# Kernel tuning notes

Measured on AMD Instinct MI355X. Metric: run time of the kernel, lower is better.

## Reference

```python
import jax, jax.numpy as jnp
import numpy as np

N, D_IN, D_OUT, H, E = 8192, 1024, 1024, 1024, 8
EPS = 0.2
S_FACTOR = 5.0


def setup_inputs() -> dict:
    key = jax.random.key(0)
    k0, k1, k2, k3 = jax.random.split(key, 4)
    x = jax.random.normal(k0, (N, D_IN), jnp.float32)
    # selector Linear(nIn, E); weights scaled by sFactor as in SMoE.__init__
    Wsel = jax.random.normal(k1, (D_IN, E), jnp.float32) * (S_FACTOR / np.sqrt(D_IN))
    bsel = jnp.zeros((E,), jnp.float32)
    # stacked 2-layer MLP experts: Linear(D_IN,H) -> ReLU -> Linear(H,D_OUT)
    W1 = jax.random.normal(k2, (E, D_IN, H), jnp.float32) / np.sqrt(D_IN)
    b1 = jnp.zeros((E, H), jnp.float32)
    W2 = jax.random.normal(k3, (E, H, D_OUT), jnp.float32) / np.sqrt(H)
    b2 = jnp.zeros((E, D_OUT), jnp.float32)
    return {"x": x, "Wsel": Wsel, "bsel": bsel, "W1": W1, "b1": b1, "W2": W2, "b2": b2}


def _sparse_weights(weightMat):
    # sort experts per token, descending (torch.sort(..., 1, descending=True))
    order = jnp.argsort(-weightMat, axis=1)                # [N,E]
    topW = jnp.take_along_axis(weightMat, order, axis=1)
    cumW = jnp.cumsum(topW, axis=1)
    capped = jnp.minimum(cumW, 1.0 - EPS)
    sw_sorted = jax.nn.relu(capped - cumW + topW)          # sparse weights, sorted order
    # softCost (side-effect metric in the original; not returned by SMoE.forward)
    shifted = jnp.pad(sw_sorted[:, 1:], ((0, 0), (0, 1)))
    _soft_cost = jnp.sum(jnp.where(shifted > 0, 1.0, sw_sorted), axis=1)
    # faithful to torch.gather(sparse_weight, 1, index) in the source
    sw = jnp.take_along_axis(sw_sorted, order, axis=1)     # [N,E]
    return sw


def reference(x, Wsel, bsel, W1, b1, W2, b2):
    weightMat = jax.nn.softmax(x @ Wsel + bsel, axis=1)    # [N,E] selector
    sw = _sparse_weights(weightMat)                        # [N,E] sparse combine weights
    # dense (vectorized) expert dispatch: tokens with sw==0 contribute 0,
    # numerically identical to the gather/scatter_add loop in sparse_MoE
    h = jax.nn.relu(jnp.einsum('nd,edh->enh', x, W1) + b1[:, None, :])   # [E,N,H]
    y = jnp.einsum('enh,eho->eno', h, W2) + b2[:, None, :]               # [E,N,O]
    out = jnp.einsum('ne,eno->no', sw, y)                                # [N,O]
    return out
```

## Files before the change

kernel.cpp:

```cpp
#include <hip/hip_runtime.h>
#include <hip/hip_bf16.h>
#include <stdint.h>

#define N_TOK 8192
#define DIN   1024
#define DOUT  1024
#define HID   1024
#define NE    8
#define CAP   0.8f

typedef __attribute__((ext_vector_type(8))) short short8;
typedef __attribute__((ext_vector_type(4))) float floatx4;

__device__ __forceinline__ void async_load16(const void* g, void* l) {
  __builtin_amdgcn_global_load_lds(
      (const __attribute__((address_space(1))) void*)g,
      (__attribute__((address_space(3))) void*)l,
      16, 0, 0);
}

__device__ __forceinline__ unsigned short bf16_bits(float f) {
  return __builtin_bit_cast(unsigned short, __float2bfloat16(f));
}

__global__ __launch_bounds__(256) void zero_kernel(float4* __restrict__ out4, int n4) {
  const int stride = gridDim.x * 256;
  for (int i = blockIdx.x * 256 + threadIdx.x; i < n4; i += stride)
    out4[i] = (float4){0.f, 0.f, 0.f, 0.f};
}

__global__ __launch_bounds__(256) void selector_kernel(
    const float* __restrict__ x, const float* __restrict__ Wsel,
    const float* __restrict__ bsel,
    __hip_bfloat16* __restrict__ x_bf, float* __restrict__ sw)
{
  const int lane = threadIdx.x & 63;
  const int wave = threadIdx.x >> 6;
  const int n = blockIdx.x * 4 + wave;
  const float4* xr4 = (const float4*)(x + (size_t)n * DIN);
  ushort4* xb4 = (ushort4*)(x_bf + (size_t)n * DIN);

  float acc[8];
#pragma unroll
  for (int e = 0; e < 8; e++) acc[e] = 0.f;

#pragma unroll
  for (int i = 0; i < 4; i++) {
    const int d4 = lane + i * 64;
    const float4 xv = xr4[d4];
    ushort4 p;
    p.x = bf16_bits(xv.x);
    p.y = bf16_bits(xv.y);
    p.z = bf16_bits(xv.z);
    p.w = bf16_bits(xv.w);
    xb4[d4] = p;
    const float xs[4] = {xv.x, xv.y, xv.z, xv.w};
#pragma unroll
    for (int q = 0; q < 4; q++) {
      const int d = d4 * 4 + q;
      const float4* wr = (const float4*)(Wsel + d * 8);
      const float4 wlo = wr[0], whi = wr[1];
      const float xv1 = xs[q];
      acc[0] += xv1 * wlo.x; acc[1] += xv1 * wlo.y;
      acc[2] += xv1 * wlo.z; acc[3] += xv1 * wlo.w;
      acc[4] += xv1 * whi.x; acc[5] += xv1 * whi.y;
      acc[6] += xv1 * whi.z; acc[7] += xv1 * whi.w;
    }
  }
#pragma unroll
  for (int off = 32; off >= 1; off >>= 1)
#pragma unroll
    for (int e = 0; e < 8; e++) acc[e] += __shfl_xor(acc[e], off);

  if (lane == 0) {
    float w[8];
    float mx = -1e30f;
#pragma unroll
    for (int e = 0; e < 8; e++) { w[e] = acc[e] + bsel[e]; mx = fmaxf(mx, w[e]); }
    float s = 0.f;
#pragma unroll
    for (int e = 0; e < 8; e++) { w[e] = expf(w[e] - mx); s += w[e]; }
    const float inv = 1.f / s;
#pragma unroll
    for (int e = 0; e < 8; e++) w[e] *= inv;

    float wsrt[8]; int ord[8];
    for (int k = 0; k < 8; k++) {
      const float v = w[k];
      int j = k;
      while (j > 0 && wsrt[j - 1] < v) { wsrt[j] = wsrt[j - 1]; ord[j] = ord[j - 1]; j--; }
      wsrt[j] = v; ord[j] = k;
    }
    float cum = 0.f, sws[8];
    for (int k = 0; k < 8; k++) {
      cum += wsrt[k];
      const float capped = fminf(cum, CAP);
      sws[k] = fmaxf(capped - cum + wsrt[k], 0.f);
    }
    for (int j = 0; j < 8; j++) sw[(size_t)n * 8 + j] = sws[ord[j]];
  }
}

__global__ __launch_bounds__(1024) void compact_kernel(
    const float* __restrict__ sw, int* __restrict__ idx, int* __restrict__ cnt)
{
  const int e = blockIdx.x;
  const int t = threadIdx.x;
  const int lane = t & 63;
  const int wv = t >> 6;
  __shared__ int wave_base[16];
  __shared__ int chunk_total;
  int base = 0;
#pragma unroll
  for (int c = 0; c < 8; c++) {
    const int tok = c * 1024 + t;
    const bool act = sw[(size_t)tok * 8 + e] > 0.f;
    const unsigned long long m = __ballot(act);
    const int before = __popcll(m & ((1ull << lane) - 1ull));
    if (lane == 0) wave_base[wv] = __popcll(m);
    __syncthreads();
    if (t == 0) {
      int s = 0;
      for (int w = 0; w < 16; w++) { const int v = wave_base[w]; wave_base[w] = s; s += v; }
      chunk_total = s;
    }
    __syncthreads();
    if (act) idx[e * N_TOK + base + wave_base[wv] + before] = tok;
    base += chunk_total;
    __syncthreads();
  }
  if (t == 0) cnt[e] = base;
}

__global__ __launch_bounds__(256) void convert_weights_kernel(
    const float* __restrict__ W1, const float* __restrict__ W2,
    __hip_bfloat16* __restrict__ W1t, __hip_bfloat16* __restrict__ W2t)
{
  __shared__ float tile[32][33];
  const int z = blockIdx.z;
  const float* src = (z & 8) ? W2 : W1;
  __hip_bfloat16* dst = (z & 8) ? W2t : W1t;
  const int e = z & 7;
  src += (size_t)e * 1024 * 1024;
  dst += (size_t)e * 1024 * 1024;
  const int R = blockIdx.y * 32, C = blockIdx.x * 32;
  const int c = threadIdx.x & 31, r0 = threadIdx.x >> 5;
#pragma unroll
  for (int p = 0; p < 4; p++) {
    const int r = r0 + p * 8;
    tile[r][c] = src[(size_t)(R + r) * 1024 + C + c];
  }
  __syncthreads();
#pragma unroll
  for (int p = 0; p < 4; p++) {
    const int r = r0 + p * 8;
    dst[(size_t)(C + r) * 1024 + R + c] = __float2bfloat16(tile[c][r]);
  }
}

#define BUFO (128 * 32)

template <int MODE>
__global__ __launch_bounds__(256, 2) void moe_gemm(
    const __hip_bfloat16* __restrict__ x_bf,
    __hip_bfloat16* __restrict__ hpool,
    const __hip_bfloat16* __restrict__ Wt,
    const float* __restrict__ biasAll,
    const float* __restrict__ sw,
    const int* __restrict__ idx, const int* __restrict__ cnt,
    float* __restrict__ out)
{
  const int e = blockIdx.z;
  const int count = cnt[e];
  const int m0 = blockIdx.y * 128;
  if (m0 >= count) return;
  const int n0 = blockIdx.x * 128;

  __shared__ __align__(16) __hip_bfloat16 sA[2 * BUFO];
  __shared__ __align__(16) __hip_bfloat16 sB[2 * BUFO];
  const int t = threadIdx.x;
  const int lane = t & 63;
  const int wave = t >> 6;
  const int wm = (wave & 1) * 64;
  const int wn = (wave >> 1) * 64;
  const int* idx_e = idx + e * N_TOK;
  const float* bias = biasAll + e * 1024;

  floatx4 acc[4][4];
#pragma unroll
  for (int i = 0; i < 4; i++)
#pragma unroll
    for (int j = 0; j < 4; j++) acc[i][j] = (floatx4){0.f, 0.f, 0.f, 0.f};

  const int sr = t >> 2;
  const int sc = (t & 3) * 8;
  const __hip_bfloat16* Ag0;
  const __hip_bfloat16* Ag1;
  if (MODE == 0) {
    const int t0 = idx_e[min(m0 + sr, count - 1)];
    const int t1 = idx_e[min(m0 + sr + 64, count - 1)];
    Ag0 = x_bf + (size_t)t0 * 1024 + sc;
    Ag1 = x_bf + (size_t)t1 * 1024 + sc;
  } else {
    const __hip_bfloat16* hp = hpool + (size_t)e * N_TOK * 1024;
    Ag0 = hp + (size_t)(m0 + sr) * 1024 + sc;
    Ag1 = hp + (size_t)(m0 + sr + 64) * 1024 + sc;
  }
  const __hip_bfloat16* Bg = Wt + (size_t)e * 1024 * 1024 + (size_t)(n0 + sr) * 1024 + sc;
  __hip_bfloat16* lA = &sA[sr * 32 + sc];
  __hip_bfloat16* lB = &sB[sr * 32 + sc];

  const int rf = lane & 15;
  const int k8 = (lane >> 4) * 8;
  const int roA = (wm + rf) * 32 + k8;
  const int roB = (wn + rf) * 32 + k8;

  async_load16(Ag0, lA);
  async_load16(Ag1, lA + 64 * 32);
  async_load16(Bg, lB);
  async_load16(Bg + (size_t)64 * 1024, lB + 64 * 32);
  __syncthreads();

#define STEP(KT, RB, WB)                                                        \
  {                                                                             \
    const int knext = ((KT) + 1) * 32;                                          \
    if (knext < 1024) {                                                         \
      async_load16(Ag0 + knext, lA + (WB) * BUFO);                              \
      async_load16(Ag1 + knext, lA + (WB) * BUFO + 64 * 32);                    \
      async_load16(Bg + knext, lB + (WB) * BUFO);                               \
      async_load16(Bg + (size_t)64 * 1024 + knext, lB + (WB) * BUFO + 64 * 32); \
    }                                                                           \
    const __hip_bfloat16* pA = &sA[(RB) * BUFO + roA];                          \
    const __hip_bfloat16* pB = &sB[(RB) * BUFO + roB];                          \
    short8 aF[4], bF[4];                                                        \
    _Pragma("unroll")                                                           \
    for (int i = 0; i < 4; i++) aF[i] = *(const short8*)(pA + i * 16 * 32);     \
    _Pragma("unroll")                                                           \
    for (int j = 0; j < 4; j++) bF[j] = *(const short8*)(pB + j * 16 * 32);     \
    _Pragma("unroll")                                                           \
    for (int i = 0; i < 4; i++)                                                 \
      _Pragma("unroll")                                                         \
      for (int j = 0; j < 4; j++)                                               \
        acc[i][j] = __builtin_amdgcn_mfma_f32_16x16x32_bf16(aF[i], bF[j],       \
                                                            acc[i][j], 0, 0, 0);\
    __syncthreads();                                                            \
  }

  for (int kt = 0; kt < 32; kt += 2) {
    STEP(kt, 0, 1);
    STEP(kt + 1, 1, 0);
  }
#undef STEP

  const int quad = lane >> 4;
  const int cn = lane & 15;
#pragma unroll
  for (int i = 0; i < 4; i++) {
#pragma unroll
    for (int r = 0; r < 4; r++) {
      const int gm = m0 + wm + i * 16 + quad * 4 + r;
      if (gm >= count) continue;
      int tok = 0; float swv = 0.f;
      if (MODE == 1) {
        tok = idx_e[gm];
        swv = sw[tok * 8 + e];
      }
#pragma unroll
      for (int j = 0; j < 4; j++) {
        const int gn = n0 + wn + j * 16 + cn;
        const float v = acc[i][j][r] + bias[gn];
        if (MODE == 0) {
          hpool[((size_t)e * N_TOK + gm) * 1024 + gn] = __float2bfloat16(fmaxf(v, 0.f));
        } else {
          unsafeAtomicAdd(&out[(size_t)tok * 1024 + gn], swv * v);
        }
      }
    }
  }
}

extern "C" void kernel_launch(void* const* d_in, const int* in_sizes, int n_in,
                              void* d_out, int out_size, void* d_ws, size_t ws_size,
                              hipStream_t stream) {
  const float* x    = (const float*)d_in[0];
  const float* Wsel = (const float*)d_in[1];
  const float* bsel = (const float*)d_in[2];
  const float* W1   = (const float*)d_in[3];
  const float* b1   = (const float*)d_in[4];
  const float* W2   = (const float*)d_in[5];
  const float* b2   = (const float*)d_in[6];
  float* out = (float*)d_out;

  char* ws = (char*)d_ws;
  __hip_bfloat16* x_bf = (__hip_bfloat16*)ws; ws += (size_t)N_TOK * DIN * 2;
  __hip_bfloat16* W1t  = (__hip_bfloat16*)ws; ws += (size_t)NE * DIN * HID * 2;
  __hip_bfloat16* W2t  = (__hip_bfloat16*)ws; ws += (size_t)NE * HID * DOUT * 2;
  float* sw            = (float*)ws;          ws += (size_t)N_TOK * NE * 4;
  int* idx             = (int*)ws;            ws += (size_t)NE * N_TOK * 4;
  int* cnt             = (int*)ws;            ws += 256;
  __hip_bfloat16* hpool = (__hip_bfloat16*)ws;

  zero_kernel<<<1024, 256, 0, stream>>>((float4*)out, N_TOK * DOUT / 4);
  selector_kernel<<<N_TOK / 4, 256, 0, stream>>>(x, Wsel, bsel, x_bf, sw);
  compact_kernel<<<NE, 1024, 0, stream>>>(sw, idx, cnt);
  convert_weights_kernel<<<dim3(32, 32, 16), 256, 0, stream>>>(W1, W2, W1t, W2t);

  moe_gemm<0><<<dim3(HID / 128, N_TOK / 128, NE), 256, 0, stream>>>(
      x_bf, hpool, W1t, b1, sw, idx, cnt, out);
  moe_gemm<1><<<dim3(DOUT / 128, N_TOK / 128, NE), 256, 0, stream>>>(
      x_bf, hpool, W2t, b2, sw, idx, cnt, out);
}
```

Baseline: 321.9 us.

## Triple-buffer LDS k-loop with explicit vmcnt waits and raw barriers

Replaces the double-buffered shared-memory pipeline in the MoE GEMM with a three-stage ring. Each stage is issued two k-steps ahead, and each compute step waits on vmcnt for only its own stage before a raw s_barrier. Launch bounds rise to 3 blocks per CU, and LDS use grows to 48KB per block. The goal is to keep more global loads in flight and hide memory latency, at the cost of more LDS per block and hand-tuned waitcnt logic that must match the load count exactly.

```diff
diff --git a/kernel.cpp b/kernel.cpp
--- a/kernel.cpp
+++ b/kernel.cpp
@@ -161,7 +161,7 @@
 #define BUFO (128 * 32)
 
 template <int MODE>
-__global__ __launch_bounds__(256, 2) void moe_gemm(
+__global__ __launch_bounds__(256, 3) void moe_gemm(
     const __hip_bfloat16* __restrict__ x_bf,
     __hip_bfloat16* __restrict__ hpool,
     const __hip_bfloat16* __restrict__ Wt,
@@ -176,8 +176,8 @@
   if (m0 >= count) return;
   const int n0 = blockIdx.x * 128;
 
-  __shared__ __align__(16) __hip_bfloat16 sA[2 * BUFO];
-  __shared__ __align__(16) __hip_bfloat16 sB[2 * BUFO];
+  __shared__ __align__(16) __hip_bfloat16 sA[3 * BUFO];
+  __shared__ __align__(16) __hip_bfloat16 sB[3 * BUFO];
   const int t = threadIdx.x;
   const int lane = t & 63;
   const int wave = t >> 6;
@@ -215,21 +215,20 @@
   const int roA = (wm + rf) * 32 + k8;
   const int roB = (wn + rf) * 32 + k8;
 
-  async_load16(Ag0, lA);
-  async_load16(Ag1, lA + 64 * 32);
-  async_load16(Bg, lB);
-  async_load16(Bg + (size_t)64 * 1024, lB + 64 * 32);
-  __syncthreads();
-
-#define STEP(KT, RB, WB)                                                        \
+#define STAGE(KT, WB)                                                           \
   {                                                                             \
-    const int knext = ((KT) + 1) * 32;                                          \
-    if (knext < 1024) {                                                         \
-      async_load16(Ag0 + knext, lA + (WB) * BUFO);                              \
-      async_load16(Ag1 + knext, lA + (WB) * BUFO + 64 * 32);                    \
-      async_load16(Bg + knext, lB + (WB) * BUFO);                               \
-      async_load16(Bg + (size_t)64 * 1024 + knext, lB + (WB) * BUFO + 64 * 32); \
-    }                                                                           \
+    const int kof = (KT) * 32;                                                  \
+    async_load16(Ag0 + kof, lA + (WB) * BUFO);                                  \
+    async_load16(Ag1 + kof, lA + (WB) * BUFO + 64 * 32);                        \
+    async_load16(Bg + kof, lB + (WB) * BUFO);                                   \
+    async_load16(Bg + (size_t)64 * 1024 + kof, lB + (WB) * BUFO + 64 * 32);     \
+  }
+
+#define GSTEP(RB, WAIT)                                                         \
+  {                                                                             \
+    asm volatile("s_waitcnt " WAIT ::: "memory");                               \
+    __builtin_amdgcn_s_barrier();                                               \
+    __builtin_amdgcn_sched_barrier(0);                                          \
     const __hip_bfloat16* pA = &sA[(RB) * BUFO + roA];                          \
     const __hip_bfloat16* pB = &sB[(RB) * BUFO + roB];                          \
     short8 aF[4], bF[4];                                                        \
@@ -243,14 +242,26 @@
       for (int j = 0; j < 4; j++)                                               \
         acc[i][j] = __builtin_amdgcn_mfma_f32_16x16x32_bf16(aF[i], bF[j],       \
                                                             acc[i][j], 0, 0, 0);\
-    __syncthreads();                                                            \
-  }
-
-  for (int kt = 0; kt < 32; kt += 2) {
-    STEP(kt, 0, 1);
-    STEP(kt + 1, 1, 0);
-  }
-#undef STEP
+    __builtin_amdgcn_s_barrier();                                               \
+    __builtin_amdgcn_sched_barrier(0);                                          \
+  }
+
+  STAGE(0, 0);
+  STAGE(1, 1);
+
+#pragma unroll 1
+  for (int kt = 0; kt < 30; kt += 3) {
+    STAGE(kt + 2, 2);
+    GSTEP(0, "vmcnt(8)");
+    STAGE(kt + 3, 0);
+    GSTEP(1, "vmcnt(8)");
+    STAGE(kt + 4, 1);
+    GSTEP(2, "vmcnt(8)");
+  }
+  GSTEP(0, "vmcnt(4)");
+  GSTEP(1, "vmcnt(0)");
+#undef GSTEP
+#undef STAGE
 
   const int quad = lane >> 4;
   const int cn = lane & 15;
@@ -278,6 +289,7 @@
     }
   }
 }
+
 
 extern "C" void kernel_launch(void* const* d_in, const int* in_sizes, int n_in,
                               void* d_out, int out_size, void* d_ws, size_t ws_size,
```

Result: slower. 345.1 us (+7.2%).

## Fuse zeroing, compaction and weight conversion kernels; remap GEMM blocks across XCDs

Applied to the files above, without the earlier changes.

The output-zeroing pass moves into the selector kernel, and token compaction runs as extra blocks of the weight-conversion launch, cutting two kernel launches and letting compaction overlap with conversion. The MoE GEMM block index is remapped so that each XCD is assigned M-blocks offset per expert, with the blocks sharing one weight tile placed together, to spread work and improve L2 reuse. The compaction blocks now use 256 threads over 32 chunks, which is more serial than the previous 1024-thread version, and they only start once they are scheduled after the z<16 blocks.

```diff
diff --git a/kernel.cpp b/kernel.cpp
--- a/kernel.cpp
+++ b/kernel.cpp
@@ -23,17 +23,19 @@
   return __builtin_bit_cast(unsigned short, __float2bfloat16(f));
 }
 
-__global__ __launch_bounds__(256) void zero_kernel(float4* __restrict__ out4, int n4) {
-  const int stride = gridDim.x * 256;
-  for (int i = blockIdx.x * 256 + threadIdx.x; i < n4; i += stride)
-    out4[i] = (float4){0.f, 0.f, 0.f, 0.f};
-}
-
 __global__ __launch_bounds__(256) void selector_kernel(
     const float* __restrict__ x, const float* __restrict__ Wsel,
     const float* __restrict__ bsel,
-    __hip_bfloat16* __restrict__ x_bf, float* __restrict__ sw)
+    __hip_bfloat16* __restrict__ x_bf, float* __restrict__ sw,
+    float4* __restrict__ out4)
 {
+  {
+    const int base = blockIdx.x * 1024 + threadIdx.x;
+    const float4 z4 = {0.f, 0.f, 0.f, 0.f};
+#pragma unroll
+    for (int r = 0; r < 4; r++) out4[base + r * 256] = z4;
+  }
+
   const int lane = threadIdx.x & 63;
   const int wave = threadIdx.x >> 6;
   const int n = blockIdx.x * 4 + wave;
@@ -101,43 +103,44 @@
   }
 }
 
-__global__ __launch_bounds__(1024) void compact_kernel(
-    const float* __restrict__ sw, int* __restrict__ idx, int* __restrict__ cnt)
-{
-  const int e = blockIdx.x;
-  const int t = threadIdx.x;
-  const int lane = t & 63;
-  const int wv = t >> 6;
-  __shared__ int wave_base[16];
-  __shared__ int chunk_total;
-  int base = 0;
-#pragma unroll
-  for (int c = 0; c < 8; c++) {
-    const int tok = c * 1024 + t;
-    const bool act = sw[(size_t)tok * 8 + e] > 0.f;
-    const unsigned long long m = __ballot(act);
-    const int before = __popcll(m & ((1ull << lane) - 1ull));
-    if (lane == 0) wave_base[wv] = __popcll(m);
-    __syncthreads();
-    if (t == 0) {
-      int s = 0;
-      for (int w = 0; w < 16; w++) { const int v = wave_base[w]; wave_base[w] = s; s += v; }
-      chunk_total = s;
-    }
-    __syncthreads();
-    if (act) idx[e * N_TOK + base + wave_base[wv] + before] = tok;
-    base += chunk_total;
-    __syncthreads();
-  }
-  if (t == 0) cnt[e] = base;
-}
-
-__global__ __launch_bounds__(256) void convert_weights_kernel(
+__global__ __launch_bounds__(256) void compact_convert_kernel(
+    const float* __restrict__ sw, int* __restrict__ idx, int* __restrict__ cnt,
     const float* __restrict__ W1, const float* __restrict__ W2,
     __hip_bfloat16* __restrict__ W1t, __hip_bfloat16* __restrict__ W2t)
 {
+  const int z = blockIdx.z;
+  if (z == 16) {
+    const int bid = blockIdx.x + 32 * blockIdx.y;
+    if (bid >= 8) return;
+    const int e = bid;
+    const int t = threadIdx.x;
+    const int lane = t & 63;
+    const int wv = t >> 6;
+    __shared__ int wave_base[4];
+    __shared__ int chunk_total;
+    int base = 0;
+    for (int c = 0; c < 32; c++) {
+      const int tok = c * 256 + t;
+      const bool act = sw[(size_t)tok * 8 + e] > 0.f;
+      const unsigned long long m = __ballot(act);
+      const int before = __popcll(m & ((1ull << lane) - 1ull));
+      if (lane == 0) wave_base[wv] = __popcll(m);
+      __syncthreads();
+      if (t == 0) {
+        int s = 0;
+        for (int w = 0; w < 4; w++) { const int v = wave_base[w]; wave_base[w] = s; s += v; }
+        chunk_total = s;
+      }
+      __syncthreads();
+      if (act) idx[e * N_TOK + base + wave_base[wv] + before] = tok;
+      base += chunk_total;
+      __syncthreads();
+    }
+    if (t == 0) cnt[e] = base;
+    return;
+  }
+
   __shared__ float tile[32][33];
-  const int z = blockIdx.z;
   const float* src = (z & 8) ? W2 : W1;
   __hip_bfloat16* dst = (z & 8) ? W2t : W1t;
   const int e = z & 7;
@@ -170,11 +173,18 @@
     const int* __restrict__ idx, const int* __restrict__ cnt,
     float* __restrict__ out)
 {
-  const int e = blockIdx.z;
+  const int lid = blockIdx.x + (blockIdx.y << 3) + (blockIdx.z << 9);
+  const int xcd = lid & 7;
+  const int s_ = lid >> 3;
+  const int nb = s_ & 7;
+  const int g  = s_ >> 3;
+  const int e  = g & 7;
+  const int mb = ((xcd - e) & 7) + ((g >> 3) << 3);
+
   const int count = cnt[e];
-  const int m0 = blockIdx.y * 128;
+  const int m0 = mb * 128;
   if (m0 >= count) return;
-  const int n0 = blockIdx.x * 128;
+  const int n0 = nb * 128;
 
   __shared__ __align__(16) __hip_bfloat16 sA[2 * BUFO];
   __shared__ __align__(16) __hip_bfloat16 sB[2 * BUFO];
@@ -300,10 +310,10 @@
   int* cnt             = (int*)ws;            ws += 256;
   __hip_bfloat16* hpool = (__hip_bfloat16*)ws;
 
-  zero_kernel<<<1024, 256, 0, stream>>>((float4*)out, N_TOK * DOUT / 4);
-  selector_kernel<<<N_TOK / 4, 256, 0, stream>>>(x, Wsel, bsel, x_bf, sw);
-  compact_kernel<<<NE, 1024, 0, stream>>>(sw, idx, cnt);
-  convert_weights_kernel<<<dim3(32, 32, 16), 256, 0, stream>>>(W1, W2, W1t, W2t);
+  selector_kernel<<<N_TOK / 4, 256, 0, stream>>>(x, Wsel, bsel, x_bf, sw,
+                                                 (float4*)out);
+  compact_convert_kernel<<<dim3(32, 32, 17), 256, 0, stream>>>(
+      sw, idx, cnt, W1, W2, W1t, W2t);
 
   moe_gemm<0><<<dim3(HID / 128, N_TOK / 128, NE), 256, 0, stream>>>(
       x_bf, hpool, W1t, b1, sw, idx, cnt, out);
```

After: 322.0 us. No clear change (+0.0%).
